# Performance work log

Hardware: AMD Instinct MI355X
Metric: run time of the kernel (lower is better)

The kernel has to match this reference:

```python
import jax, jax.numpy as jnp
import numpy as np

N_NODES = 100000
EMB_DIM = 128
EDGE_FEAT_DIM = 16
N_EDGES = 1000000
HIDDEN = 64


def setup_inputs() -> dict:
    key = jax.random.key(0)
    k1, k2, k3, k4, k5 = jax.random.split(key, 5)
    z = jax.random.normal(k1, (N_NODES, EMB_DIM), dtype=jnp.float32)
    edge_index = jax.random.randint(k2, (2, N_EDGES), 0, N_NODES, dtype=jnp.int64)
    edge_attr = jax.random.normal(k3, (N_EDGES, EDGE_FEAT_DIM), dtype=jnp.float32)
    fan_in1 = 2 * EMB_DIM + EDGE_FEAT_DIM
    W1 = jax.random.normal(k4, (fan_in1, HIDDEN), dtype=jnp.float32) / np.sqrt(fan_in1)
    b1 = jnp.zeros((HIDDEN,), dtype=jnp.float32)
    W2 = jax.random.normal(k5, (HIDDEN, 1), dtype=jnp.float32) / np.sqrt(HIDDEN)
    b2 = jnp.zeros((1,), dtype=jnp.float32)
    return {"z": z, "edge_index": edge_index, "edge_attr": edge_attr,
            "W1": W1, "b1": b1, "W2": W2, "b2": b2}


def reference(z, edge_index, edge_attr, W1, b1, W2, b2):
    src = z[edge_index[0]]  # [E, emb_dim]
    dst = z[edge_index[1]]  # [E, emb_dim]
    x = jnp.concatenate([src, dst, edge_attr], axis=1)  # [E, 2*emb+feat]
    h = jax.nn.relu(x @ W1 + b1)  # [E, 64]
    return jax.nn.sigmoid(h @ W2 + b2).squeeze(-1)  # [E]
```

## Files before the change

### kernel.cpp

```cpp
#include <hip/hip_runtime.h>
#include <hip/hip_bf16.h>
#include <math.h>

#define EMB   128
#define ATTR  16
#define KDIM  272
#define KPAD  288
#define HID   64

typedef short s16x8 __attribute__((ext_vector_type(8)));
typedef float f32x4 __attribute__((ext_vector_type(4)));

union FragB { ushort s[8]; uint4 q; s16x8 v; };
union FragA { __hip_bfloat162 h2[4]; s16x8 v; };

static __device__ __forceinline__ ushort f2bf(float f) {
    union { float f; uint u; } v; v.f = f;
    uint u = v.u;
    return (ushort)((u + 0x7FFFu + ((u >> 16) & 1u)) >> 16);
}

__global__ void prep_w1t(const float* __restrict__ W1, ushort* __restrict__ w1t) {
    int idx = blockIdx.x * blockDim.x + threadIdx.x;
    int j = idx / KPAD;
    int k = idx - j * KPAD;
    float v = (k < KDIM) ? W1[k * HID + j] : 0.f;
    w1t[idx] = f2bf(v);
}

__global__ __launch_bounds__(256, 4)
void edge_mlp_blds(const float* __restrict__ z,
                   const int*   __restrict__ eidx,
                   const float* __restrict__ attr,
                   const ushort* __restrict__ w1t,
                   const float* __restrict__ b1,
                   const float* __restrict__ w2,
                   const float* __restrict__ b2,
                   float*       __restrict__ out,
                   int E, int n_nodes)
{
    __shared__ ushort blds[HID * KPAD];

    const int tid = threadIdx.x;

    {
        const uint4* __restrict__ src = reinterpret_cast<const uint4*>(w1t);
        uint4* dst = reinterpret_cast<uint4*>(blds);
        #pragma unroll
        for (int i = 0; i < 9; ++i) dst[tid + i * 256] = src[tid + i * 256];
    }
    __syncthreads();

    const int lane = tid & 63;
    const int wv   = tid >> 6;
    const int rl   = lane & 15;
    const int kh   = lane >> 4;

    const int ebase = (blockIdx.x * 4 + wv) * 32;
    int eg0 = ebase + rl;        if (eg0 >= E) eg0 = E - 1;
    int eg1 = ebase + 16 + rl;   if (eg1 >= E) eg1 = E - 1;

    int si0 = eidx[eg0];      if ((unsigned)si0 >= (unsigned)n_nodes) si0 = 0;
    int di0 = eidx[E + eg0];  if ((unsigned)di0 >= (unsigned)n_nodes) di0 = 0;
    int si1 = eidx[eg1];      if ((unsigned)si1 >= (unsigned)n_nodes) si1 = 0;
    int di1 = eidx[E + eg1];  if ((unsigned)di1 >= (unsigned)n_nodes) di1 = 0;

    const float4* __restrict__ sp0 = reinterpret_cast<const float4*>(z + (size_t)si0 * EMB);
    const float4* __restrict__ dp0 = reinterpret_cast<const float4*>(z + (size_t)di0 * EMB);
    const float4* __restrict__ ap0 = reinterpret_cast<const float4*>(attr + (size_t)eg0 * ATTR);
    const float4* __restrict__ sp1 = reinterpret_cast<const float4*>(z + (size_t)si1 * EMB);
    const float4* __restrict__ dp1 = reinterpret_cast<const float4*>(z + (size_t)di1 * EMB);
    const float4* __restrict__ ap1 = reinterpret_cast<const float4*>(attr + (size_t)eg1 * ATTR);
    const ushort* __restrict__ bp  = blds + rl * KPAD + kh * 8;

    f32x4 acc[2][4];
    #pragma unroll
    for (int rb = 0; rb < 2; ++rb)
        #pragma unroll
        for (int nf = 0; nf < 4; ++nf) acc[rb][nf] = (f32x4){0.f, 0.f, 0.f, 0.f};

    #pragma unroll
    for (int s = 0; s < 9; ++s) {
        float4 f00, f01, f10, f11;
        if (s < 4) {
            f00 = sp0[s * 8 + kh * 2]; f01 = sp0[s * 8 + kh * 2 + 1];
            f10 = sp1[s * 8 + kh * 2]; f11 = sp1[s * 8 + kh * 2 + 1];
        } else if (s < 8) {
            f00 = dp0[(s - 4) * 8 + kh * 2]; f01 = dp0[(s - 4) * 8 + kh * 2 + 1];
            f10 = dp1[(s - 4) * 8 + kh * 2]; f11 = dp1[(s - 4) * 8 + kh * 2 + 1];
        } else if (kh < 2) {
            f00 = ap0[kh * 2]; f01 = ap0[kh * 2 + 1];
            f10 = ap1[kh * 2]; f11 = ap1[kh * 2 + 1];
        } else {
            f00 = make_float4(0.f, 0.f, 0.f, 0.f); f01 = f00; f10 = f00; f11 = f00;
        }
        FragA a0, a1;
        a0.h2[0] = __float22bfloat162_rn(make_float2(f00.x, f00.y));
        a0.h2[1] = __float22bfloat162_rn(make_float2(f00.z, f00.w));
        a0.h2[2] = __float22bfloat162_rn(make_float2(f01.x, f01.y));
        a0.h2[3] = __float22bfloat162_rn(make_float2(f01.z, f01.w));
        a1.h2[0] = __float22bfloat162_rn(make_float2(f10.x, f10.y));
        a1.h2[1] = __float22bfloat162_rn(make_float2(f10.z, f10.w));
        a1.h2[2] = __float22bfloat162_rn(make_float2(f11.x, f11.y));
        a1.h2[3] = __float22bfloat162_rn(make_float2(f11.z, f11.w));

        #pragma unroll
        for (int nf = 0; nf < 4; ++nf) {
            FragB b;
            b.q = *reinterpret_cast<const uint4*>(bp + nf * 16 * KPAD + s * 32);
            acc[0][nf] = __builtin_amdgcn_mfma_f32_16x16x32_bf16(a0.v, b.v, acc[0][nf], 0, 0, 0);
            acc[1][nf] = __builtin_amdgcn_mfma_f32_16x16x32_bf16(a1.v, b.v, acc[1][nf], 0, 0, 0);
        }
    }

    const float bb2 = b2[0];
    #pragma unroll
    for (int rb = 0; rb < 2; ++rb) {
        float p[4] = {0.f, 0.f, 0.f, 0.f};
        #pragma unroll
        for (int nf = 0; nf < 4; ++nf) {
            const int j = nf * 16 + rl;
            const float bb = b1[j];
            const float ww = w2[j];
            #pragma unroll
            for (int r = 0; r < 4; ++r) {
                float h = acc[rb][nf][r] + bb;
                h = fmaxf(h, 0.f);
                p[r] = fmaf(h, ww, p[r]);
            }
        }
        #pragma unroll
        for (int m = 1; m <= 8; m <<= 1) {
            #pragma unroll
            for (int r = 0; r < 4; ++r) p[r] += __shfl_xor(p[r], m, 64);
        }
        if (rl == 0) {
            const int eout = ebase + rb * 16 + kh * 4;
            #pragma unroll
            for (int r = 0; r < 4; ++r) {
                if (eout + r < E) {
                    const float sv = p[r] + bb2;
                    out[eout + r] = 1.f / (1.f + expf(-sv));
                }
            }
        }
    }
}

extern "C" void kernel_launch(void* const* d_in, const int* in_sizes, int n_in,
                              void* d_out, int out_size, void* d_ws, size_t ws_size,
                              hipStream_t stream)
{
    const float* z  = (const float*)d_in[0];
    const int*   ei = (const int*)  d_in[1];
    const float* ea = (const float*)d_in[2];
    const float* W1 = (const float*)d_in[3];
    const float* b1 = (const float*)d_in[4];
    const float* W2 = (const float*)d_in[5];
    const float* b2 = (const float*)d_in[6];
    float* out = (float*)d_out;

    const int E       = in_sizes[1] / 2;
    const int n_nodes = in_sizes[0] / EMB;

    ushort* w1t = (ushort*)d_ws;

    hipLaunchKernelGGL(prep_w1t, dim3((HID * KPAD) / 256), dim3(256), 0, stream, W1, w1t);

    const int grid = (E + 127) / 128;
    hipLaunchKernelGGL(edge_mlp_blds, dim3(grid), dim3(256), 0, stream,
                       z, ei, ea, w1t, b1, W2, b2, out, E, n_nodes);
}
```

Baseline: 268.7 us.

## Pre-convert node embeddings to bf16 table so edge gathers read half the bytes

Adds a prep pass that converts the whole z table to bf16 in workspace, fused with the W1 transpose into one launch. The edge kernel then gathers bf16 rows directly into MFMA A fragments with one 16-byte load per step, halving gather traffic and dropping per-edge conversions. The cost is an extra full read of z (51MB) and a write of 25MB each call. A fallback keeps the old path when the workspace is too small.

```diff
diff --git a/kernel.cpp b/kernel.cpp
--- a/kernel.cpp
+++ b/kernel.cpp
@@ -12,7 +12,7 @@
 typedef float f32x4 __attribute__((ext_vector_type(4)));
 
 union FragB { ushort s[8]; uint4 q; s16x8 v; };
-union FragA { __hip_bfloat162 h2[4]; s16x8 v; };
+union FragA { __hip_bfloat162 h2[4]; uint4 q; s16x8 v; };
 
 static __device__ __forceinline__ ushort f2bf(float f) {
     union { float f; uint u; } v; v.f = f;
@@ -20,12 +20,151 @@
     return (ushort)((u + 0x7FFFu + ((u >> 16) & 1u)) >> 16);
 }
 
-__global__ void prep_w1t(const float* __restrict__ W1, ushort* __restrict__ w1t) {
-    int idx = blockIdx.x * blockDim.x + threadIdx.x;
-    int j = idx / KPAD;
-    int k = idx - j * KPAD;
-    float v = (k < KDIM) ? W1[k * HID + j] : 0.f;
-    w1t[idx] = f2bf(v);
+__global__ void prep_all(const float* __restrict__ z, ushort* __restrict__ zb,
+                         const float* __restrict__ W1, ushort* __restrict__ w1t,
+                         int nzb, int n_z)
+{
+    const int bid = blockIdx.x;
+    if (bid < nzb) {
+        const int i = bid * 256 + threadIdx.x;
+        const int e0 = i * 8;
+        if (e0 + 8 <= n_z) {
+            const float4* src = reinterpret_cast<const float4*>(z + e0);
+            float4 f0 = src[0], f1 = src[1];
+            FragA pk;
+            pk.h2[0] = __float22bfloat162_rn(make_float2(f0.x, f0.y));
+            pk.h2[1] = __float22bfloat162_rn(make_float2(f0.z, f0.w));
+            pk.h2[2] = __float22bfloat162_rn(make_float2(f1.x, f1.y));
+            pk.h2[3] = __float22bfloat162_rn(make_float2(f1.z, f1.w));
+            *reinterpret_cast<uint4*>(zb + e0) = pk.q;
+        }
+    } else {
+        const int idx = (bid - nzb) * 256 + threadIdx.x;
+        const int j = idx / KPAD;
+        const int k = idx - j * KPAD;
+        if (j < HID) {
+            float v = (k < KDIM) ? W1[k * HID + j] : 0.f;
+            w1t[idx] = f2bf(v);
+        }
+    }
+}
+
+__global__ __launch_bounds__(256, 4)
+void edge_mlp_zb(const ushort* __restrict__ zb,
+                 const int*   __restrict__ eidx,
+                 const float* __restrict__ attr,
+                 const ushort* __restrict__ w1t,
+                 const float* __restrict__ b1,
+                 const float* __restrict__ w2,
+                 const float* __restrict__ b2,
+                 float*       __restrict__ out,
+                 int E, int n_nodes)
+{
+    __shared__ ushort blds[HID * KPAD];
+
+    const int tid = threadIdx.x;
+    {
+        const uint4* __restrict__ src = reinterpret_cast<const uint4*>(w1t);
+        uint4* dst = reinterpret_cast<uint4*>(blds);
+        #pragma unroll
+        for (int i = 0; i < 9; ++i) dst[tid + i * 256] = src[tid + i * 256];
+    }
+    __syncthreads();
+
+    const int lane = tid & 63;
+    const int wv   = tid >> 6;
+    const int rl   = lane & 15;
+    const int kh   = lane >> 4;
+
+    const int ebase = (blockIdx.x * 4 + wv) * 32;
+    int eg0 = ebase + rl;        if (eg0 >= E) eg0 = E - 1;
+    int eg1 = ebase + 16 + rl;   if (eg1 >= E) eg1 = E - 1;
+
+    int si0 = eidx[eg0];      if ((unsigned)si0 >= (unsigned)n_nodes) si0 = 0;
+    int di0 = eidx[E + eg0];  if ((unsigned)di0 >= (unsigned)n_nodes) di0 = 0;
+    int si1 = eidx[eg1];      if ((unsigned)si1 >= (unsigned)n_nodes) si1 = 0;
+    int di1 = eidx[E + eg1];  if ((unsigned)di1 >= (unsigned)n_nodes) di1 = 0;
+
+    const ushort* __restrict__ sp0 = zb + (size_t)si0 * EMB;
+    const ushort* __restrict__ dp0 = zb + (size_t)di0 * EMB;
+    const ushort* __restrict__ sp1 = zb + (size_t)si1 * EMB;
+    const ushort* __restrict__ dp1 = zb + (size_t)di1 * EMB;
+    const float4* __restrict__ ap0 = reinterpret_cast<const float4*>(attr + (size_t)eg0 * ATTR);
+    const float4* __restrict__ ap1 = reinterpret_cast<const float4*>(attr + (size_t)eg1 * ATTR);
+    const ushort* __restrict__ bp  = blds + rl * KPAD + kh * 8;
+
+    f32x4 acc[2][4];
+    #pragma unroll
+    for (int rb = 0; rb < 2; ++rb)
+        #pragma unroll
+        for (int nf = 0; nf < 4; ++nf) acc[rb][nf] = (f32x4){0.f, 0.f, 0.f, 0.f};
+
+    #pragma unroll
+    for (int s = 0; s < 9; ++s) {
+        FragA a0, a1;
+        if (s < 4) {
+            a0.q = *reinterpret_cast<const uint4*>(sp0 + s * 32 + kh * 8);
+            a1.q = *reinterpret_cast<const uint4*>(sp1 + s * 32 + kh * 8);
+        } else if (s < 8) {
+            a0.q = *reinterpret_cast<const uint4*>(dp0 + (s - 4) * 32 + kh * 8);
+            a1.q = *reinterpret_cast<const uint4*>(dp1 + (s - 4) * 32 + kh * 8);
+        } else if (kh < 2) {
+            float4 f00 = ap0[kh * 2], f01 = ap0[kh * 2 + 1];
+            float4 f10 = ap1[kh * 2], f11 = ap1[kh * 2 + 1];
+            a0.h2[0] = __float22bfloat162_rn(make_float2(f00.x, f00.y));
+            a0.h2[1] = __float22bfloat162_rn(make_float2(f00.z, f00.w));
+            a0.h2[2] = __float22bfloat162_rn(make_float2(f01.x, f01.y));
+            a0.h2[3] = __float22bfloat162_rn(make_float2(f01.z, f01.w));
+            a1.h2[0] = __float22bfloat162_rn(make_float2(f10.x, f10.y));
+            a1.h2[1] = __float22bfloat162_rn(make_float2(f10.z, f10.w));
+            a1.h2[2] = __float22bfloat162_rn(make_float2(f11.x, f11.y));
+            a1.h2[3] = __float22bfloat162_rn(make_float2(f11.z, f11.w));
+        } else {
+            a0.q = make_uint4(0u, 0u, 0u, 0u);
+            a1.q = make_uint4(0u, 0u, 0u, 0u);
+        }
+
+        #pragma unroll
+        for (int nf = 0; nf < 4; ++nf) {
+            FragB b;
+            b.q = *reinterpret_cast<const uint4*>(bp + nf * 16 * KPAD + s * 32);
+            acc[0][nf] = __builtin_amdgcn_mfma_f32_16x16x32_bf16(a0.v, b.v, acc[0][nf], 0, 0, 0);
+            acc[1][nf] = __builtin_amdgcn_mfma_f32_16x16x32_bf16(a1.v, b.v, acc[1][nf], 0, 0, 0);
+        }
+    }
+
+    const float bb2 = b2[0];
+    #pragma unroll
+    for (int rb = 0; rb < 2; ++rb) {
+        float p[4] = {0.f, 0.f, 0.f, 0.f};
+        #pragma unroll
+        for (int nf = 0; nf < 4; ++nf) {
+            const int j = nf * 16 + rl;
+            const float bb = b1[j];
+            const float ww = w2[j];
+            #pragma unroll
+            for (int r = 0; r < 4; ++r) {
+                float h = acc[rb][nf][r] + bb;
+                h = fmaxf(h, 0.f);
+                p[r] = fmaf(h, ww, p[r]);
+            }
+        }
+        #pragma unroll
+        for (int m = 1; m <= 8; m <<= 1) {
+            #pragma unroll
+            for (int r = 0; r < 4; ++r) p[r] += __shfl_xor(p[r], m, 64);
+        }
+        if (rl == 0) {
+            const int eout = ebase + rb * 16 + kh * 4;
+            #pragma unroll
+            for (int r = 0; r < 4; ++r) {
+                if (eout + r < E) {
+                    const float sv = p[r] + bb2;
+                    out[eout + r] = 1.f / (1.f + expf(-sv));
+                }
+            }
+        }
+    }
 }
 
 __global__ __launch_bounds__(256, 4)
@@ -40,9 +179,7 @@
                    int E, int n_nodes)
 {
     __shared__ ushort blds[HID * KPAD];
-
     const int tid = threadIdx.x;
-
     {
         const uint4* __restrict__ src = reinterpret_cast<const uint4*>(w1t);
         uint4* dst = reinterpret_cast<uint4*>(blds);
@@ -147,6 +284,14 @@
     }
 }
 
+__global__ void prep_w1t_only(const float* __restrict__ W1, ushort* __restrict__ w1t) {
+    int idx = blockIdx.x * blockDim.x + threadIdx.x;
+    int j = idx / KPAD;
+    int k = idx - j * KPAD;
+    float v = (k < KDIM) ? W1[k * HID + j] : 0.f;
+    w1t[idx] = f2bf(v);
+}
+
 extern "C" void kernel_launch(void* const* d_in, const int* in_sizes, int n_in,
                               void* d_out, int out_size, void* d_ws, size_t ws_size,
                               hipStream_t stream)
@@ -162,12 +307,25 @@
 
     const int E       = in_sizes[1] / 2;
     const int n_nodes = in_sizes[0] / EMB;
+    const int n_z     = n_nodes * EMB;
 
     ushort* w1t = (ushort*)d_ws;
-
-    hipLaunchKernelGGL(prep_w1t, dim3((HID * KPAD) / 256), dim3(256), 0, stream, W1, w1t);
+    ushort* zb  = (ushort*)d_ws + HID * KPAD;
+    const size_t needed = (size_t)HID * KPAD * 2 + (size_t)n_z * 2;
 
     const int grid = (E + 127) / 128;
-    hipLaunchKernelGGL(edge_mlp_blds, dim3(grid), dim3(256), 0, stream,
-                       z, ei, ea, w1t, b1, W2, b2, out, E, n_nodes);
-}
+
+    if (ws_size >= needed) {
+        const int nzb = (n_z / 8 + 255) / 256;
+        const int wblk = (HID * KPAD + 255) / 256;
+        hipLaunchKernelGGL(prep_all, dim3(nzb + wblk), dim3(256), 0, stream,
+                           z, zb, W1, w1t, nzb, n_z);
+        hipLaunchKernelGGL(edge_mlp_zb, dim3(grid), dim3(256), 0, stream,
+                           zb, ei, ea, w1t, b1, W2, b2, out, E, n_nodes);
+    } else {
+        hipLaunchKernelGGL(prep_w1t_only, dim3((HID * KPAD) / 256), dim3(256), 0, stream,
+                           W1, w1t);
+        hipLaunchKernelGGL(edge_mlp_blds, dim3(grid), dim3(256), 0, stream,
+                           z, ei, ea, w1t, b1, W2, b2, out, E, n_nodes);
+    }
+}
```

Result: faster. 221.3 us (-17.6%).
